# Performance work log

Hardware: AMD Instinct MI355X
Metric: run time of the kernel (lower is better)

Reference implementation:

```python
import jax, jax.numpy as jnp
import numpy as np

D_ATT = 256
D_GROUP = 32
N_GROUP = D_ATT // D_GROUP


def setup_inputs() -> dict:
    key = jax.random.key(0)
    ks = jax.random.split(key, 6)
    B, L = 4, 512
    import math
    s = 1.0 / math.sqrt(D_ATT)
    return {
        "x": jax.random.normal(ks[0], (B, L, D_ATT), dtype=jnp.float32),
        "Wq": jax.random.normal(ks[1], (D_ATT, D_ATT), dtype=jnp.float32) * s * 0.06,
        "Wk": jax.random.normal(ks[2], (D_ATT, D_ATT), dtype=jnp.float32) * s * 0.06,
        "Wv": jax.random.normal(ks[3], (D_ATT, D_ATT), dtype=jnp.float32) * s * 0.06,
        "w_mlp": jax.random.normal(ks[4], (D_GROUP,), dtype=jnp.float32) * 0.1,
        "b_mlp": jax.random.normal(ks[5], (1,), dtype=jnp.float32) * 0.1,
    }


def reference(x, Wq, Wk, Wv, w_mlp, b_mlp):
    B, L, d_att = x.shape
    G, Dg = N_GROUP, D_GROUP
    # nn.Linear(bias=False): y = x @ W.T
    Q = x @ Wq.T  # (B, L, d_att)
    K = x @ Wk.T
    V = x @ Wv.T
    Qg = Q.reshape(B, L, 1, G, Dg)
    Kg = K.reshape(B, 1, L, G, Dg)
    # group_MLP: ReLU -> Linear(Dg, 1) -> ReLU, applied to Q-K diff
    # diff: (B, Lq, Lk, G, Dg) -- the huge intermediate a fused kernel would avoid
    diff = Qg - Kg
    attn = jnp.einsum('bqkgd,d->bqkg', jax.nn.relu(diff), w_mlp) + b_mlp[0]
    attn = jax.nn.relu(attn)
    # positional_adding_bias=0, positional_multiplying_bias=1 (defaults), no mask
    attn = jax.nn.softmax(attn, axis=2)  # softmax over key positions
    # NOTE: original views V as (B, L, d_group, n_group) -- asymmetric grouping, kept faithful
    Vg = V.reshape(B, L, Dg, G)
    out = jnp.einsum('bqkg,bkdg->bqdg', attn, Vg)  # (B, Lq, Dg, G)
    return out.reshape(B, L, d_att)
```

## Files before the change

kernel.cpp:

```cpp
#include <hip/hip_runtime.h>

typedef float f32x2 __attribute__((ext_vector_type(2)));
typedef float f32x4 __attribute__((ext_vector_type(4)));
typedef _Float16 h16x2 __attribute__((ext_vector_type(2)));
typedef _Float16 h16x4 __attribute__((ext_vector_type(4)));
typedef _Float16 h16x8 __attribute__((ext_vector_type(8)));

#define LL 512
#define M_ROWS 2048

#if __has_builtin(__builtin_amdgcn_exp2f)
#define EXP2F __builtin_amdgcn_exp2f
#else
#define EXP2F exp2f
#endif
#define LOG2E 1.44269504088896340736f

__device__ __forceinline__ float quad_swap1(float x) {
    return __int_as_float(__builtin_amdgcn_mov_dpp(__float_as_int(x), 0xB1, 0xF, 0xF, true));
}
__device__ __forceinline__ float quad_swap2(float x) {
    return __int_as_float(__builtin_amdgcn_mov_dpp(__float_as_int(x), 0x4E, 0xF, 0xF, true));
}

__device__ __forceinline__ float fdot2f(h16x2 a, h16x2 b, float c) {
#if __has_builtin(__builtin_amdgcn_fdot2)
    return __builtin_amdgcn_fdot2(a, b, c, false);
#else
    return fmaf((float)a.x, (float)b.x, fmaf((float)a.y, (float)b.y, c));
#endif
}

__global__ __launch_bounds__(128) void qkv_gemm(
    const float* __restrict__ X, const float* __restrict__ Wq,
    const float* __restrict__ Wk, const float* __restrict__ Wv,
    _Float16* __restrict__ Qh, _Float16* __restrict__ Kh, float* __restrict__ Vt)
{
    const int bx = blockIdx.x;
    const int by = blockIdx.y;
    const int mat = bx >> 2;
    const int n0 = (bx & 3) * 64;
    const int m0 = by * 32;
    const float* W = (mat == 0) ? Wq : (mat == 1 ? Wk : Wv);

    __shared__ float As[2][32][36];
    __shared__ float Bs[2][32][68];

    const int t = threadIdx.x;
    const int tx = t & 15;
    const int ty = t >> 4;

    int am[2], ak4[2];
#pragma unroll
    for (int r = 0; r < 2; ++r) { int idx = t + 128 * r; am[r] = idx >> 3; ak4[r] = idx & 7; }
    int bn[4], bk4[4]; size_t brow[4];
#pragma unroll
    for (int r = 0; r < 4; ++r) {
        int idx = t + 128 * r; bn[r] = idx >> 3; bk4[r] = idx & 7;
        int rowc = n0 + bn[r];
        brow[r] = (mat == 2) ? (size_t)(((rowc & 31) << 3) | (rowc >> 5)) : (size_t)rowc;
    }

    f32x4 arg[2], brg[4];
    auto load_tile = [&](int kc) {
#pragma unroll
        for (int r = 0; r < 2; ++r)
            arg[r] = *(const f32x4*)(X + (size_t)(m0 + am[r]) * 256 + kc + ak4[r] * 4);
#pragma unroll
        for (int r = 0; r < 4; ++r)
            brg[r] = *(const f32x4*)(W + brow[r] * 256 + kc + bk4[r] * 4);
    };
    auto store_tile = [&](int buf) {
#pragma unroll
        for (int r = 0; r < 2; ++r)
#pragma unroll
            for (int j = 0; j < 4; ++j) As[buf][ak4[r] * 4 + j][am[r]] = arg[r][j];
#pragma unroll
        for (int r = 0; r < 4; ++r)
#pragma unroll
            for (int j = 0; j < 4; ++j) Bs[buf][bk4[r] * 4 + j][bn[r]] = brg[r][j];
    };

    load_tile(0);
    store_tile(0);
    __syncthreads();

    f32x2 c[4][2];
#pragma unroll
    for (int i = 0; i < 4; ++i) { c[i][0] = (f32x2){0.f, 0.f}; c[i][1] = (f32x2){0.f, 0.f}; }

    for (int it = 0; it < 8; ++it) {
        const int buf = it & 1;
        if (it < 7) load_tile((it + 1) * 32);
#pragma unroll
        for (int kk = 0; kk < 32; ++kk) {
            const f32x4 a4 = *(const f32x4*)&As[buf][kk][ty * 4];
            const f32x4 b4 = *(const f32x4*)&Bs[buf][kk][tx * 4];
            const f32x2 bl = __builtin_shufflevector(b4, b4, 0, 1);
            const f32x2 bh = __builtin_shufflevector(b4, b4, 2, 3);
#pragma unroll
            for (int i = 0; i < 4; ++i) {
                const f32x2 ai = {a4[i], a4[i]};
                c[i][0] += ai * bl;
                c[i][1] += ai * bh;
            }
        }
        if (it < 7) {
            __syncthreads();
            store_tile(buf ^ 1);
            __syncthreads();
        }
    }

    const int colb = n0 + tx * 4;
    if (mat == 2) {
#pragma unroll
        for (int i = 0; i < 4; ++i) {
            f32x4 v = {c[i][0].x, c[i][0].y, c[i][1].x, c[i][1].y};
            *(f32x4*)(Vt + (size_t)(m0 + ty * 4 + i) * 256 + colb) = v;
        }
    } else {
        _Float16* Hb = (mat == 0) ? Qh : Kh;
#pragma unroll
        for (int i = 0; i < 4; ++i) {
            h16x4 hv = {(_Float16)c[i][0].x, (_Float16)c[i][0].y,
                        (_Float16)c[i][1].x, (_Float16)c[i][1].y};
            *(h16x4*)(Hb + (size_t)(m0 + ty * 4 + i) * 256 + colb) = hv;
        }
    }
}

__global__ __launch_bounds__(1024, 4) void attn_fused(
    const _Float16* __restrict__ Qh, const _Float16* __restrict__ Kh,
    const float* __restrict__ Vt,
    const float* __restrict__ w_mlp, const float* __restrict__ b_mlp,
    float* __restrict__ out)
{
    const int bid = blockIdx.x;
    const int b = bid & 3;
    const int q0 = (bid >> 2) * 8;

    const int t = threadIdx.x;
    const int p = t >> 6;
    const int lane64 = t & 63;
    const int half = (t >> 5) & 1;
    const int lane32 = t & 31;
    const int dh = t & 3;
    const int g = lane32 >> 2;

    __shared__ float accbuf[16][64][34];

    const int doff = g * 32 + dh * 8;
    const float bias4 = b_mlp[0] * (LOG2E * 0.25f);
    const bool odd = (dh & 1) != 0;
    const bool hi  = (dh & 2) != 0;

    h16x2 w2[4];
    {
        f32x4 wa = *(const f32x4*)(w_mlp + dh * 8);
        f32x4 wb = *(const f32x4*)(w_mlp + dh * 8 + 4);
        wa *= LOG2E; wb *= LOG2E;
        w2[0] = (h16x2){(_Float16)wa.x, (_Float16)wa.y};
        w2[1] = (h16x2){(_Float16)wa.z, (_Float16)wa.w};
        w2[2] = (h16x2){(_Float16)wb.x, (_Float16)wb.y};
        w2[3] = (h16x2){(_Float16)wb.z, (_Float16)wb.w};
    }

    h16x2 qr2[4][4];
#pragma unroll
    for (int q = 0; q < 4; ++q) {
        const h16x8 qv = *(const h16x8*)(Qh + ((size_t)(b * LL) + q0 + half * 4 + q) * 256 + doff);
        qr2[q][0] = __builtin_shufflevector(qv, qv, 0, 1);
        qr2[q][1] = __builtin_shufflevector(qv, qv, 2, 3);
        qr2[q][2] = __builtin_shufflevector(qv, qv, 4, 5);
        qr2[q][3] = __builtin_shufflevector(qv, qv, 6, 7);
    }

    f32x2 acc2[4][4];
#pragma unroll
    for (int s = 0; s < 4; ++s)
#pragma unroll
        for (int j = 0; j < 4; ++j) acc2[s][j] = (f32x2){0.f, 0.f};
    float lown = 0.f;

    const _Float16* kptr = Kh + ((size_t)(b * LL) + p) * 256 + doff;
    const float* vptr = Vt + ((size_t)(b * LL) + p) * 256 + doff;

    const h16x2 zh = {(_Float16)0.f, (_Float16)0.f};

    auto compute = [&](h16x8 kv, f32x4 va, f32x4 vb) {
        h16x2 k2[4] = {__builtin_shufflevector(kv, kv, 0, 1),
                       __builtin_shufflevector(kv, kv, 2, 3),
                       __builtin_shufflevector(kv, kv, 4, 5),
                       __builtin_shufflevector(kv, kv, 6, 7)};
        f32x2 v2[4] = {__builtin_shufflevector(va, va, 0, 1),
                       __builtin_shufflevector(va, va, 2, 3),
                       __builtin_shufflevector(vb, vb, 0, 1),
                       __builtin_shufflevector(vb, vb, 2, 3)};
        float ps[4];
#pragma unroll
        for (int q = 0; q < 4; ++q) {
            float s = bias4;
#pragma unroll
            for (int j = 0; j < 4; ++j) {
                h16x2 d2 = qr2[q][j] - k2[j];
                h16x2 r2 = __builtin_elementwise_max(d2, zh);
                s = fdot2f(w2[j], r2, s);
            }
            ps[q] = s;
        }
        const float r01 = quad_swap1(odd ? ps[0] : ps[1]);
        const float z01 = (odd ? ps[1] : ps[0]) + r01;
        const float r23 = quad_swap1(odd ? ps[2] : ps[3]);
        const float z23 = (odd ? ps[3] : ps[2]) + r23;
        const float r2f = quad_swap2(hi ? z01 : z23);
        const float zz  = (hi ? z23 : z01) + r2f;
        const float sfull = fmaxf(zz, 0.f);
        const float e = EXP2F(sfull);
        lown += e;
        const float e1 = quad_swap1(e);
        const float e2 = quad_swap2(e);
        const float e3 = quad_swap2(e1);
        const float es[4] = {e, e1, e2, e3};
#pragma unroll
        for (int s = 0; s < 4; ++s) {
            const f32x2 ee = {es[s], es[s]};
#pragma unroll
            for (int j = 0; j < 4; ++j)
                acc2[s][j] = __builtin_elementwise_fma(v2[j], ee, acc2[s][j]);
        }
    };

    h16x8 k0 = *(const h16x8*)kptr;
    f32x4 va0 = *(const f32x4*)vptr, vb0 = *(const f32x4*)(vptr + 4);
    kptr += 16 * 256; vptr += 16 * 256;
    h16x8 k1 = *(const h16x8*)kptr;
    f32x4 va1 = *(const f32x4*)vptr, vb1 = *(const f32x4*)(vptr + 4);

#pragma unroll 1
    for (int i = 0; i < 15; ++i) {
        kptr += 16 * 256; vptr += 16 * 256;
        h16x8 k2n = *(const h16x8*)kptr;
        f32x4 va2n = *(const f32x4*)vptr, vb2n = *(const f32x4*)(vptr + 4);
        compute(k0, va0, vb0);
        kptr += 16 * 256; vptr += 16 * 256;
        h16x8 k3n = *(const h16x8*)kptr;
        f32x4 va3n = *(const f32x4*)vptr, vb3n = *(const f32x4*)(vptr + 4);
        compute(k1, va1, vb1);
        k0 = k2n; va0 = va2n; vb0 = vb2n;
        k1 = k3n; va1 = va3n; vb1 = vb3n;
    }
    compute(k0, va0, vb0);
    compute(k1, va1, vb1);

    {
        float* rowp = &accbuf[p][lane64][0];
#pragma unroll
        for (int s = 0; s < 4; ++s)
#pragma unroll
            for (int j = 0; j < 4; ++j)
                *(f32x2*)(rowp + s * 8 + j * 2) = acc2[s][j];
        rowp[32] = lown;
    }
    __syncthreads();

#pragma unroll
    for (int r = 0; r < 2; ++r) {
        const int o = t + 1024 * r;
        const int q = o >> 8;
        const int c = o & 255;
        const int gs = c & 7;
        const int dd = c >> 3;
        const int dhs = dd >> 3;
        const int rem = dd & 7;
        const int s = dhs ^ (q & 3);
        const int lsrc = (q >> 2) * 32 + gs * 4 + dhs;
        const int lden = (q >> 2) * 32 + gs * 4 + (q & 3);
        float sum = 0.f, den = 0.f;
#pragma unroll
        for (int pp = 0; pp < 16; ++pp) {
            sum += accbuf[pp][lsrc][s * 8 + rem];
            den += accbuf[pp][lden][32];
        }
        out[((size_t)(b * LL) + q0 + q) * 256 + c] = sum / den;
    }
}

extern "C" void kernel_launch(void* const* d_in, const int* in_sizes, int n_in,
                              void* d_out, int out_size, void* d_ws, size_t ws_size,
                              hipStream_t stream) {
    (void)in_sizes; (void)n_in; (void)out_size; (void)ws_size;
    const float* x     = (const float*)d_in[0];
    const float* Wq    = (const float*)d_in[1];
    const float* Wk    = (const float*)d_in[2];
    const float* Wv    = (const float*)d_in[3];
    const float* w_mlp = (const float*)d_in[4];
    const float* b_mlp = (const float*)d_in[5];
    float* outp = (float*)d_out;

    _Float16* Qh = (_Float16*)d_ws;
    _Float16* Kh = (_Float16*)((char*)d_ws + (size_t)1048576);
    float*    Vt = (float*)((char*)d_ws + (size_t)2097152);

    qkv_gemm<<<dim3(12, 64), 128, 0, stream>>>(x, Wq, Wk, Wv, Qh, Kh, Vt);
    attn_fused<<<dim3(256), 1024, 0, stream>>>(Qh, Kh, Vt, w_mlp, b_mlp, outp);
}
```

Before: 111.0 us.

## Fuse QKV GEMM and attention into one cooperative kernel with grid sync

Merges the QKV projection GEMM and the attention kernel into a single cooperative launch. Each 1024-thread block first runs three 128-thread GEMM sub-tiles while the remaining threads idle, then a grid-wide sync precedes the attention phase. Shared memory is a union reused by both phases. This removes one kernel launch and the gap between the two kernels, at the cost of leaving most threads idle during the GEMM phase and paying for a grid barrier.

```diff
diff --git a/kernel.cpp b/kernel.cpp
--- a/kernel.cpp
+++ b/kernel.cpp
@@ -1,4 +1,7 @@
 #include <hip/hip_runtime.h>
+#include <hip/hip_cooperative_groups.h>
+
+namespace cg = cooperative_groups;
 
 typedef float f32x2 __attribute__((ext_vector_type(2)));
 typedef float f32x4 __attribute__((ext_vector_type(4)));
@@ -7,7 +10,6 @@
 typedef _Float16 h16x8 __attribute__((ext_vector_type(8)));
 
 #define LL 512
-#define M_ROWS 2048
 
 #if __has_builtin(__builtin_amdgcn_exp2f)
 #define EXP2F __builtin_amdgcn_exp2f
@@ -31,258 +33,266 @@
 #endif
 }
 
-__global__ __launch_bounds__(128) void qkv_gemm(
+union Smem {
+    struct { float As[3][2][32][36]; float Bs[3][2][32][68]; } g;
+    float accbuf[16][64][34];
+};
+
+__global__ __launch_bounds__(1024, 4) void fused_all(
     const float* __restrict__ X, const float* __restrict__ Wq,
     const float* __restrict__ Wk, const float* __restrict__ Wv,
-    _Float16* __restrict__ Qh, _Float16* __restrict__ Kh, float* __restrict__ Vt)
-{
-    const int bx = blockIdx.x;
-    const int by = blockIdx.y;
-    const int mat = bx >> 2;
-    const int n0 = (bx & 3) * 64;
-    const int m0 = by * 32;
-    const float* W = (mat == 0) ? Wq : (mat == 1 ? Wk : Wv);
-
-    __shared__ float As[2][32][36];
-    __shared__ float Bs[2][32][68];
-
-    const int t = threadIdx.x;
-    const int tx = t & 15;
-    const int ty = t >> 4;
-
-    int am[2], ak4[2];
-#pragma unroll
-    for (int r = 0; r < 2; ++r) { int idx = t + 128 * r; am[r] = idx >> 3; ak4[r] = idx & 7; }
-    int bn[4], bk4[4]; size_t brow[4];
-#pragma unroll
-    for (int r = 0; r < 4; ++r) {
-        int idx = t + 128 * r; bn[r] = idx >> 3; bk4[r] = idx & 7;
-        int rowc = n0 + bn[r];
-        brow[r] = (mat == 2) ? (size_t)(((rowc & 31) << 3) | (rowc >> 5)) : (size_t)rowc;
-    }
-
-    f32x4 arg[2], brg[4];
-    auto load_tile = [&](int kc) {
-#pragma unroll
-        for (int r = 0; r < 2; ++r)
-            arg[r] = *(const f32x4*)(X + (size_t)(m0 + am[r]) * 256 + kc + ak4[r] * 4);
-#pragma unroll
-        for (int r = 0; r < 4; ++r)
-            brg[r] = *(const f32x4*)(W + brow[r] * 256 + kc + bk4[r] * 4);
-    };
-    auto store_tile = [&](int buf) {
-#pragma unroll
-        for (int r = 0; r < 2; ++r)
-#pragma unroll
-            for (int j = 0; j < 4; ++j) As[buf][ak4[r] * 4 + j][am[r]] = arg[r][j];
-#pragma unroll
-        for (int r = 0; r < 4; ++r)
-#pragma unroll
-            for (int j = 0; j < 4; ++j) Bs[buf][bk4[r] * 4 + j][bn[r]] = brg[r][j];
-    };
-
-    load_tile(0);
-    store_tile(0);
-    __syncthreads();
-
-    f32x2 c[4][2];
-#pragma unroll
-    for (int i = 0; i < 4; ++i) { c[i][0] = (f32x2){0.f, 0.f}; c[i][1] = (f32x2){0.f, 0.f}; }
-
-    for (int it = 0; it < 8; ++it) {
-        const int buf = it & 1;
-        if (it < 7) load_tile((it + 1) * 32);
-#pragma unroll
-        for (int kk = 0; kk < 32; ++kk) {
-            const f32x4 a4 = *(const f32x4*)&As[buf][kk][ty * 4];
-            const f32x4 b4 = *(const f32x4*)&Bs[buf][kk][tx * 4];
-            const f32x2 bl = __builtin_shufflevector(b4, b4, 0, 1);
-            const f32x2 bh = __builtin_shufflevector(b4, b4, 2, 3);
-#pragma unroll
-            for (int i = 0; i < 4; ++i) {
-                const f32x2 ai = {a4[i], a4[i]};
-                c[i][0] += ai * bl;
-                c[i][1] += ai * bh;
-            }
-        }
-        if (it < 7) {
-            __syncthreads();
-            store_tile(buf ^ 1);
-            __syncthreads();
-        }
-    }
-
-    const int colb = n0 + tx * 4;
-    if (mat == 2) {
-#pragma unroll
-        for (int i = 0; i < 4; ++i) {
-            f32x4 v = {c[i][0].x, c[i][0].y, c[i][1].x, c[i][1].y};
-            *(f32x4*)(Vt + (size_t)(m0 + ty * 4 + i) * 256 + colb) = v;
-        }
-    } else {
-        _Float16* Hb = (mat == 0) ? Qh : Kh;
-#pragma unroll
-        for (int i = 0; i < 4; ++i) {
-            h16x4 hv = {(_Float16)c[i][0].x, (_Float16)c[i][0].y,
-                        (_Float16)c[i][1].x, (_Float16)c[i][1].y};
-            *(h16x4*)(Hb + (size_t)(m0 + ty * 4 + i) * 256 + colb) = hv;
-        }
-    }
-}
-
-__global__ __launch_bounds__(1024, 4) void attn_fused(
-    const _Float16* __restrict__ Qh, const _Float16* __restrict__ Kh,
-    const float* __restrict__ Vt,
     const float* __restrict__ w_mlp, const float* __restrict__ b_mlp,
+    _Float16* __restrict__ Qh, _Float16* __restrict__ Kh, float* __restrict__ Vt,
     float* __restrict__ out)
 {
+    __shared__ Smem sm;
     const int bid = blockIdx.x;
-    const int b = bid & 3;
-    const int q0 = (bid >> 2) * 8;
-
     const int t = threadIdx.x;
-    const int p = t >> 6;
-    const int lane64 = t & 63;
-    const int half = (t >> 5) & 1;
-    const int lane32 = t & 31;
-    const int dh = t & 3;
-    const int g = lane32 >> 2;
-
-    __shared__ float accbuf[16][64][34];
-
-    const int doff = g * 32 + dh * 8;
-    const float bias4 = b_mlp[0] * (LOG2E * 0.25f);
-    const bool odd = (dh & 1) != 0;
-    const bool hi  = (dh & 2) != 0;
-
-    h16x2 w2[4];
+
     {
-        f32x4 wa = *(const f32x4*)(w_mlp + dh * 8);
-        f32x4 wb = *(const f32x4*)(w_mlp + dh * 8 + 4);
-        wa *= LOG2E; wb *= LOG2E;
-        w2[0] = (h16x2){(_Float16)wa.x, (_Float16)wa.y};
-        w2[1] = (h16x2){(_Float16)wa.z, (_Float16)wa.w};
-        w2[2] = (h16x2){(_Float16)wb.x, (_Float16)wb.y};
-        w2[3] = (h16x2){(_Float16)wb.z, (_Float16)wb.w};
+        const int sb = t >> 7;
+        const bool act = (sb < 3);
+        const int lt = t & 127;
+        const int T = bid * 3 + sb;
+        const int mat = T >> 8;
+        const int n0 = ((T >> 6) & 3) * 64;
+        const int m0 = (T & 63) * 32;
+        const float* W = (mat == 0) ? Wq : (mat == 1 ? Wk : Wv);
+
+        const int tx = lt & 15;
+        const int ty = lt >> 4;
+
+        int am[2], ak4[2];
+#pragma unroll
+        for (int r = 0; r < 2; ++r) { int idx = lt + 128 * r; am[r] = idx >> 3; ak4[r] = idx & 7; }
+        int bn[4], bk4[4]; size_t brow[4];
+#pragma unroll
+        for (int r = 0; r < 4; ++r) {
+            int idx = lt + 128 * r; bn[r] = idx >> 3; bk4[r] = idx & 7;
+            int rowc = n0 + bn[r];
+            brow[r] = (mat == 2) ? (size_t)(((rowc & 31) << 3) | (rowc >> 5)) : (size_t)rowc;
+        }
+
+        f32x4 arg[2], brg[4];
+        auto load_tile = [&](int kc) {
+#pragma unroll
+            for (int r = 0; r < 2; ++r)
+                arg[r] = *(const f32x4*)(X + (size_t)(m0 + am[r]) * 256 + kc + ak4[r] * 4);
+#pragma unroll
+            for (int r = 0; r < 4; ++r)
+                brg[r] = *(const f32x4*)(W + brow[r] * 256 + kc + bk4[r] * 4);
+        };
+        auto store_tile = [&](int buf) {
+#pragma unroll
+            for (int r = 0; r < 2; ++r)
+#pragma unroll
+                for (int j = 0; j < 4; ++j) sm.g.As[sb][buf][ak4[r] * 4 + j][am[r]] = arg[r][j];
+#pragma unroll
+            for (int r = 0; r < 4; ++r)
+#pragma unroll
+                for (int j = 0; j < 4; ++j) sm.g.Bs[sb][buf][bk4[r] * 4 + j][bn[r]] = brg[r][j];
+        };
+
+        if (act) { load_tile(0); store_tile(0); }
+        __syncthreads();
+
+        f32x2 c[4][2];
+#pragma unroll
+        for (int i = 0; i < 4; ++i) { c[i][0] = (f32x2){0.f, 0.f}; c[i][1] = (f32x2){0.f, 0.f}; }
+
+        for (int it = 0; it < 8; ++it) {
+            const int buf = it & 1;
+            if (act) {
+                if (it < 7) load_tile((it + 1) * 32);
+#pragma unroll
+                for (int kk = 0; kk < 32; ++kk) {
+                    const f32x4 a4 = *(const f32x4*)&sm.g.As[sb][buf][kk][ty * 4];
+                    const f32x4 b4 = *(const f32x4*)&sm.g.Bs[sb][buf][kk][tx * 4];
+                    const f32x2 bl = __builtin_shufflevector(b4, b4, 0, 1);
+                    const f32x2 bh = __builtin_shufflevector(b4, b4, 2, 3);
+#pragma unroll
+                    for (int i = 0; i < 4; ++i) {
+                        const f32x2 ai = {a4[i], a4[i]};
+                        c[i][0] += ai * bl;
+                        c[i][1] += ai * bh;
+                    }
+                }
+            }
+            if (it < 7) {
+                __syncthreads();
+                if (act) store_tile(buf ^ 1);
+                __syncthreads();
+            }
+        }
+
+        if (act) {
+            const int colb = n0 + tx * 4;
+            if (mat == 2) {
+#pragma unroll
+                for (int i = 0; i < 4; ++i) {
+                    f32x4 v = {c[i][0].x, c[i][0].y, c[i][1].x, c[i][1].y};
+                    *(f32x4*)(Vt + (size_t)(m0 + ty * 4 + i) * 256 + colb) = v;
+                }
+            } else {
+                _Float16* Hb = (mat == 0) ? Qh : Kh;
+#pragma unroll
+                for (int i = 0; i < 4; ++i) {
+                    h16x4 hv = {(_Float16)c[i][0].x, (_Float16)c[i][0].y,
+                                (_Float16)c[i][1].x, (_Float16)c[i][1].y};
+                    *(h16x4*)(Hb + (size_t)(m0 + ty * 4 + i) * 256 + colb) = hv;
+                }
+            }
+        }
     }
 
-    h16x2 qr2[4][4];
-#pragma unroll
-    for (int q = 0; q < 4; ++q) {
-        const h16x8 qv = *(const h16x8*)(Qh + ((size_t)(b * LL) + q0 + half * 4 + q) * 256 + doff);
-        qr2[q][0] = __builtin_shufflevector(qv, qv, 0, 1);
-        qr2[q][1] = __builtin_shufflevector(qv, qv, 2, 3);
-        qr2[q][2] = __builtin_shufflevector(qv, qv, 4, 5);
-        qr2[q][3] = __builtin_shufflevector(qv, qv, 6, 7);
-    }
-
-    f32x2 acc2[4][4];
-#pragma unroll
-    for (int s = 0; s < 4; ++s)
-#pragma unroll
-        for (int j = 0; j < 4; ++j) acc2[s][j] = (f32x2){0.f, 0.f};
-    float lown = 0.f;
-
-    const _Float16* kptr = Kh + ((size_t)(b * LL) + p) * 256 + doff;
-    const float* vptr = Vt + ((size_t)(b * LL) + p) * 256 + doff;
-
-    const h16x2 zh = {(_Float16)0.f, (_Float16)0.f};
-
-    auto compute = [&](h16x8 kv, f32x4 va, f32x4 vb) {
-        h16x2 k2[4] = {__builtin_shufflevector(kv, kv, 0, 1),
-                       __builtin_shufflevector(kv, kv, 2, 3),
-                       __builtin_shufflevector(kv, kv, 4, 5),
-                       __builtin_shufflevector(kv, kv, 6, 7)};
-        f32x2 v2[4] = {__builtin_shufflevector(va, va, 0, 1),
-                       __builtin_shufflevector(va, va, 2, 3),
-                       __builtin_shufflevector(vb, vb, 0, 1),
-                       __builtin_shufflevector(vb, vb, 2, 3)};
-        float ps[4];
+    cg::this_grid().sync();
+
+    {
+        const int b = bid & 3;
+        const int q0 = (bid >> 2) * 8;
+
+        const int p = t >> 6;
+        const int lane64 = t & 63;
+        const int half = (t >> 5) & 1;
+        const int lane32 = t & 31;
+        const int dh = t & 3;
+        const int g = lane32 >> 2;
+
+        const int doff = g * 32 + dh * 8;
+        const float bias4 = b_mlp[0] * (LOG2E * 0.25f);
+        const bool odd = (dh & 1) != 0;
+        const bool hi  = (dh & 2) != 0;
+
+        h16x2 w2[4];
+        {
+            f32x4 wa = *(const f32x4*)(w_mlp + dh * 8);
+            f32x4 wb = *(const f32x4*)(w_mlp + dh * 8 + 4);
+            wa *= LOG2E; wb *= LOG2E;
+            w2[0] = (h16x2){(_Float16)wa.x, (_Float16)wa.y};
+            w2[1] = (h16x2){(_Float16)wa.z, (_Float16)wa.w};
+            w2[2] = (h16x2){(_Float16)wb.x, (_Float16)wb.y};
+            w2[3] = (h16x2){(_Float16)wb.z, (_Float16)wb.w};
+        }
+
+        h16x2 qr2[4][4];
 #pragma unroll
         for (int q = 0; q < 4; ++q) {
-            float s = bias4;
-#pragma unroll
-            for (int j = 0; j < 4; ++j) {
-                h16x2 d2 = qr2[q][j] - k2[j];
-                h16x2 r2 = __builtin_elementwise_max(d2, zh);
-                s = fdot2f(w2[j], r2, s);
-            }
-            ps[q] = s;
-        }
-        const float r01 = quad_swap1(odd ? ps[0] : ps[1]);
-        const float z01 = (odd ? ps[1] : ps[0]) + r01;
-        const float r23 = quad_swap1(odd ? ps[2] : ps[3]);
-        const float z23 = (odd ? ps[3] : ps[2]) + r23;
-        const float r2f = quad_swap2(hi ? z01 : z23);
-        const float zz  = (hi ? z23 : z01) + r2f;
-        const float sfull = fmaxf(zz, 0.f);
-        const float e = EXP2F(sfull);
-        lown += e;
-        const float e1 = quad_swap1(e);
-        const float e2 = quad_swap2(e);
-        const float e3 = quad_swap2(e1);
-        const float es[4] = {e, e1, e2, e3};
-#pragma unroll
-        for (int s = 0; s < 4; ++s) {
-            const f32x2 ee = {es[s], es[s]};
-#pragma unroll
-            for (int j = 0; j < 4; ++j)
-                acc2[s][j] = __builtin_elementwise_fma(v2[j], ee, acc2[s][j]);
-        }
-    };
-
-    h16x8 k0 = *(const h16x8*)kptr;
-    f32x4 va0 = *(const f32x4*)vptr, vb0 = *(const f32x4*)(vptr + 4);
-    kptr += 16 * 256; vptr += 16 * 256;
-    h16x8 k1 = *(const h16x8*)kptr;
-    f32x4 va1 = *(const f32x4*)vptr, vb1 = *(const f32x4*)(vptr + 4);
+            const h16x8 qv = *(const h16x8*)(Qh + ((size_t)(b * LL) + q0 + half * 4 + q) * 256 + doff);
+            qr2[q][0] = __builtin_shufflevector(qv, qv, 0, 1);
+            qr2[q][1] = __builtin_shufflevector(qv, qv, 2, 3);
+            qr2[q][2] = __builtin_shufflevector(qv, qv, 4, 5);
+            qr2[q][3] = __builtin_shufflevector(qv, qv, 6, 7);
+        }
+
+        f32x2 acc2[4][4];
+#pragma unroll
+        for (int s = 0; s < 4; ++s)
+#pragma unroll
+            for (int j = 0; j < 4; ++j) acc2[s][j] = (f32x2){0.f, 0.f};
+        float lown = 0.f;
+
+        const _Float16* kptr = Kh + ((size_t)(b * LL) + p) * 256 + doff;
+        const float* vptr = Vt + ((size_t)(b * LL) + p) * 256 + doff;
+
+        const h16x2 zh = {(_Float16)0.f, (_Float16)0.f};
+
+        auto compute = [&](h16x8 kv, f32x4 va, f32x4 vb) {
+            h16x2 k2[4] = {__builtin_shufflevector(kv, kv, 0, 1),
+                           __builtin_shufflevector(kv, kv, 2, 3),
+                           __builtin_shufflevector(kv, kv, 4, 5),
+                           __builtin_shufflevector(kv, kv, 6, 7)};
+            f32x2 v2[4] = {__builtin_shufflevector(va, va, 0, 1),
+                           __builtin_shufflevector(va, va, 2, 3),
+                           __builtin_shufflevector(vb, vb, 0, 1),
+                           __builtin_shufflevector(vb, vb, 2, 3)};
+            float ps[4];
+#pragma unroll
+            for (int q = 0; q < 4; ++q) {
+                float s = bias4;
+#pragma unroll
+                for (int j = 0; j < 4; ++j) {
+                    h16x2 d2 = qr2[q][j] - k2[j];
+                    h16x2 r2 = __builtin_elementwise_max(d2, zh);
+                    s = fdot2f(w2[j], r2, s);
+                }
+                ps[q] = s;
+            }
+            const float r01 = quad_swap1(odd ? ps[0] : ps[1]);
+            const float z01 = (odd ? ps[1] : ps[0]) + r01;
+            const float r23 = quad_swap1(odd ? ps[2] : ps[3]);
+            const float z23 = (odd ? ps[3] : ps[2]) + r23;
+            const float r2f = quad_swap2(hi ? z01 : z23);
+            const float zz  = (hi ? z23 : z01) + r2f;
+            const float sfull = fmaxf(zz, 0.f);
+            const float e = EXP2F(sfull);
+            lown += e;
+            const float e1 = quad_swap1(e);
+            const float e2 = quad_swap2(e);
+            const float e3 = quad_swap2(e1);
+            const float es[4] = {e, e1, e2, e3};
+#pragma unroll
+            for (int s = 0; s < 4; ++s) {
+                const f32x2 ee = {es[s], es[s]};
+#pragma unroll
+                for (int j = 0; j < 4; ++j)
+                    acc2[s][j] = __builtin_elementwise_fma(v2[j], ee, acc2[s][j]);
+            }
+        };
+
+        h16x8 k0 = *(const h16x8*)kptr;
+        f32x4 va0 = *(const f32x4*)vptr, vb0 = *(const f32x4*)(vptr + 4);
+        kptr += 16 * 256; vptr += 16 * 256;
+        h16x8 k1 = *(const h16x8*)kptr;
+        f32x4 va1 = *(const f32x4*)vptr, vb1 = *(const f32x4*)(vptr + 4);
 
 #pragma unroll 1
-    for (int i = 0; i < 15; ++i) {
-        kptr += 16 * 256; vptr += 16 * 256;
-        h16x8 k2n = *(const h16x8*)kptr;
-        f32x4 va2n = *(const f32x4*)vptr, vb2n = *(const f32x4*)(vptr + 4);
+        for (int i = 0; i < 15; ++i) {
+            kptr += 16 * 256; vptr += 16 * 256;
+            h16x8 k2n = *(const h16x8*)kptr;
+            f32x4 va2n = *(const f32x4*)vptr, vb2n = *(const f32x4*)(vptr + 4);
+            compute(k0, va0, vb0);
+            kptr += 16 * 256; vptr += 16 * 256;
+            h16x8 k3n = *(const h16x8*)kptr;
+            f32x4 va3n = *(const f32x4*)vptr, vb3n = *(const f32x4*)(vptr + 4);
+            compute(k1, va1, vb1);
+            k0 = k2n; va0 = va2n; vb0 = vb2n;
+            k1 = k3n; va1 = va3n; vb1 = vb3n;
+        }
         compute(k0, va0, vb0);
-        kptr += 16 * 256; vptr += 16 * 256;
-        h16x8 k3n = *(const h16x8*)kptr;
-        f32x4 va3n = *(const f32x4*)vptr, vb3n = *(const f32x4*)(vptr + 4);
         compute(k1, va1, vb1);
-        k0 = k2n; va0 = va2n; vb0 = vb2n;
-        k1 = k3n; va1 = va3n; vb1 = vb3n;
-    }
-    compute(k0, va0, vb0);
-    compute(k1, va1, vb1);
-
-    {
-        float* rowp = &accbuf[p][lane64][0];
-#pragma unroll
-        for (int s = 0; s < 4; ++s)
-#pragma unroll
-            for (int j = 0; j < 4; ++j)
-                *(f32x2*)(rowp + s * 8 + j * 2) = acc2[s][j];
-        rowp[32] = lown;
-    }
-    __syncthreads();
-
-#pragma unroll
-    for (int r = 0; r < 2; ++r) {
-        const int o = t + 1024 * r;
-        const int q = o >> 8;
-        const int c = o & 255;
-        const int gs = c & 7;
-        const int dd = c >> 3;
-        const int dhs = dd >> 3;
-        const int rem = dd & 7;
-        const int s = dhs ^ (q & 3);
-        const int lsrc = (q >> 2) * 32 + gs * 4 + dhs;
-        const int lden = (q >> 2) * 32 + gs * 4 + (q & 3);
-        float sum = 0.f, den = 0.f;
-#pragma unroll
-        for (int pp = 0; pp < 16; ++pp) {
-            sum += accbuf[pp][lsrc][s * 8 + rem];
-            den += accbuf[pp][lden][32];
-        }
-        out[((size_t)(b * LL) + q0 + q) * 256 + c] = sum / den;
+
+        __syncthreads();
+        {
+            float* rowp = &sm.accbuf[p][lane64][0];
+#pragma unroll
+            for (int s = 0; s < 4; ++s)
+#pragma unroll
+                for (int j = 0; j < 4; ++j)
+                    *(f32x2*)(rowp + s * 8 + j * 2) = acc2[s][j];
+            rowp[32] = lown;
+        }
+        __syncthreads();
+
+#pragma unroll
+        for (int r = 0; r < 2; ++r) {
+            const int o = t + 1024 * r;
+            const int q = o >> 8;
+            const int c = o & 255;
+            const int gs = c & 7;
+            const int dd = c >> 3;
+            const int dhs = dd >> 3;
+            const int rem = dd & 7;
+            const int s = dhs ^ (q & 3);
+            const int lsrc = (q >> 2) * 32 + gs * 4 + dhs;
+            const int lden = (q >> 2) * 32 + gs * 4 + (q & 3);
+            float sum = 0.f, den = 0.f;
+#pragma unroll
+            for (int pp = 0; pp < 16; ++pp) {
+                sum += sm.accbuf[pp][lsrc][s * 8 + rem];
+                den += sm.accbuf[pp][lden][32];
+            }
+            out[((size_t)(b * LL) + q0 + q) * 256 + c] = sum / den;
+        }
     }
 }
 
@@ -302,6 +312,11 @@
     _Float16* Kh = (_Float16*)((char*)d_ws + (size_t)1048576);
     float*    Vt = (float*)((char*)d_ws + (size_t)2097152);
 
-    qkv_gemm<<<dim3(12, 64), 128, 0, stream>>>(x, Wq, Wk, Wv, Qh, Kh, Vt);
-    attn_fused<<<dim3(256), 1024, 0, stream>>>(Qh, Kh, Vt, w_mlp, b_mlp, outp);
-}
+    void* kargs[] = {
+        (void*)&x, (void*)&Wq, (void*)&Wk, (void*)&Wv,
+        (void*)&w_mlp, (void*)&b_mlp,
+        (void*)&Qh, (void*)&Kh, (void*)&Vt, (void*)&outp
+    };
+    hipLaunchCooperativeKernel((const void*)fused_all, dim3(256), dim3(1024),
+                               kargs, 0, stream);
+}
```

Measured after the change: 165.8 us. 49.3% more time.
